# Optimization experiments

Hardware: AMD Instinct MI355X
Metric: run time of the kernel (lower is better)

## Reference

```python
import jax, jax.numpy as jnp
import numpy as np
import math

B, H, S, D, P = 1, 8, 512, 64, 32  # batch, heads, seq, d_k, proj_dim


def setup_inputs() -> dict:
    key = jax.random.key(0)
    ks = jax.random.split(key, 9)
    mu = math.log(math.sqrt(2.0 / D))  # PositiveLinear raw init mean

    def raw(k):
        return mu + 0.2 * jax.random.normal(k, (D, D), jnp.float32)

    return dict(
        q=jax.random.normal(ks[0], (B, H, S, D), jnp.float32),
        k=jax.random.normal(ks[1], (B, H, S, D), jnp.float32),
        v=jax.random.normal(ks[2], (B, H, S, D), jnp.float32),
        sq_raw1=raw(ks[3]), sq_b1=jnp.zeros((D,), jnp.float32),
        sq_raw2=raw(ks[4]), sq_b2=jnp.zeros((D,), jnp.float32),
        sk_raw1=raw(ks[5]), sk_b1=jnp.zeros((D,), jnp.float32),
        sk_raw2=raw(ks[6]), sk_b2=jnp.zeros((D,), jnp.float32),
        Wh=jax.random.normal(ks[7], (P, D), jnp.float32) / jnp.sqrt(jnp.float32(D)),
        Wv=jax.random.normal(ks[8], (P, D), jnp.float32) / jnp.sqrt(jnp.float32(D)),
    )


def _icnn(x, r1, b1, r2, b2):
    # Input-convex net: positive weights via softplus, softplus activations.
    z = jax.nn.softplus(x @ jax.nn.softplus(r1).T + b1)
    z = jax.nn.softplus(z @ jax.nn.softplus(r2).T + b2)
    return z.sum(-1)  # scalar convex score per token: [B,H,S]


def reference(q, k, v, sq_raw1, sq_b1, sq_raw2, sq_b2,
              sk_raw1, sk_b1, sk_raw2, sk_b2, Wh, Wv):
    f_q = _icnn(q, sq_raw1, sq_b1, sq_raw2, sq_b2)  # [B,H,S]
    g_k = _icnn(k, sk_raw1, sk_b1, sk_raw2, sk_b2)  # [B,H,S]
    phi_q = jnp.exp(q @ Wh.T)  # [B,H,S,P]
    phi_k = jnp.exp(k @ Wh.T)  # [B,H,S,P]
    scores = jnp.einsum('bhsr,bhtr->bhst', phi_q, phi_k)  # [B,H,S,S], strictly positive
    s_ij = f_q[..., :, None] + g_k[..., None, :] + jnp.log(scores)  # [B,H,S,S]
    u = v @ Wv.T  # [B,H,S,P] (index t)
    Sz = s_ij.shape[-1]
    # y[bhsp] = logsumexp_t(s_ij[bhst] + u[bhtp]) - log S, computed without the 5D tensor:
    m1 = jax.lax.stop_gradient(jnp.max(s_ij, axis=-1, keepdims=True))  # [B,H,S,1]
    m2 = jax.lax.stop_gradient(jnp.max(u, axis=2, keepdims=True))      # [B,H,1,P]
    acc = jnp.einsum('bhst,bhtp->bhsp', jnp.exp(s_ij - m1), jnp.exp(u - m2))
    y = jnp.log(acc) + m1 + m2 - jnp.log(jnp.float32(Sz))
    return y  # [B,H,S,P]
```

## Files before the change

kernel.cpp:

```cpp
#include <hip/hip_runtime.h>
#include <math.h>

#define HH 8
#define SS 512
#define DD 64
#define PP 32


__device__ __forceinline__ float softplusf(float x) {
    if (x > 20.f) return x;
    return log1pf(__expf(x));
}

__global__ __launch_bounds__(256) void csm_prep(
    const float* __restrict__ sq1, const float* __restrict__ sq2,
    const float* __restrict__ sk1, const float* __restrict__ sk2,
    const float* __restrict__ Wh, const float* __restrict__ Wv,
    float* __restrict__ wbuf)
{
    int idx = blockIdx.x * 256 + threadIdx.x;
    if (idx < 16384) {
        int m = idx >> 12, r = idx & 4095;
        int i = r >> 6, j = r & 63;
        const float* src = (m == 0) ? sq1 : (m == 1) ? sq2 : (m == 2) ? sk1 : sk2;
        wbuf[idx] = softplusf(src[j * 64 + i]);
    } else if (idx < 18432) {
        int r = idx - 16384; int i = r >> 5, p = r & 31;
        wbuf[idx] = Wh[p * 64 + i];
    } else if (idx < 20480) {
        int r = idx - 18432; int i = r >> 5, p = r & 31;
        wbuf[idx] = Wv[p * 64 + i];
    }
}

__global__ __launch_bounds__(256) void csm_token3(
    const float* __restrict__ q, const float* __restrict__ k, const float* __restrict__ v,
    const float* __restrict__ sq_b1, const float* __restrict__ sq_b2,
    const float* __restrict__ sk_b1, const float* __restrict__ sk_b2,
    const float* __restrict__ wbuf,
    float* __restrict__ fq, float* __restrict__ gk, float* __restrict__ gkpart,
    float* __restrict__ phiq, float* __restrict__ phik, float* __restrict__ uexp)
{
    __shared__ float xs[32 * 68];
    __shared__ float wb[64 * 68];
    __shared__ float wh[64 * 36];
    __shared__ float part[32 * 17];
    __shared__ float bb1[64], bb2[64];

    const int bx   = blockIdx.x;
    const int role = bx >> 7;
    const int sub  = bx & 127;
    const int g0   = sub * 32;
    const int tid  = threadIdx.x;
    const int tr = tid >> 4, tc = tid & 15;
    const int m0 = tr * 2, n0 = tc * 4, p0 = tc * 2;

    const float* xin = (role == 0) ? q : (role == 1) ? k : v;

    const float4* xsrc = (const float4*)(xin + g0 * 64);
    #pragma unroll
    for (int c = 0; c < 2; ++c) {
        int idx4 = tid + c * 256;
        int t = idx4 >> 4, ic = (idx4 & 15) * 4;
        *(float4*)&xs[t * 68 + ic] = xsrc[idx4];
    }
    const float4* whsrc = (const float4*)(wbuf + ((role == 2) ? 18432 : 16384));
    #pragma unroll
    for (int c = 0; c < 2; ++c) {
        int idx4 = tid + c * 256;
        int i = idx4 >> 3, pc = (idx4 & 7) * 4;
        *(float4*)&wh[i * 36 + pc] = whsrc[idx4];
    }
    if (role < 2) {
        const float4* w1src = (const float4*)(wbuf + (role == 0 ? 0 : 8192));
        #pragma unroll
        for (int c = 0; c < 4; ++c) {
            int idx4 = tid + c * 256;
            int i = idx4 >> 4, jc = (idx4 & 15) * 4;
            *(float4*)&wb[i * 68 + jc] = w1src[idx4];
        }
        if (tid < 64)       bb1[tid]      = (role == 0 ? sq_b1 : sk_b1)[tid];
        else if (tid < 128) bb2[tid - 64] = (role == 0 ? sq_b2 : sk_b2)[tid - 64];
    }
    __syncthreads();

    if (role == 2) {
        float acc[2][2] = {{0.f,0.f},{0.f,0.f}};
        #pragma unroll
        for (int kc = 0; kc < 16; ++kc) {
            const int i0 = kc * 4;
            float4 xv[2]; float2 hv[4];
            xv[0] = *(const float4*)&xs[(m0 + 0) * 68 + i0];
            xv[1] = *(const float4*)&xs[(m0 + 1) * 68 + i0];
            #pragma unroll
            for (int kk = 0; kk < 4; ++kk) hv[kk] = *(const float2*)&wh[(i0 + kk) * 36 + p0];
            #pragma unroll
            for (int mm = 0; mm < 2; ++mm) {
                const float* xa = (const float*)&xv[mm];
                #pragma unroll
                for (int kk = 0; kk < 4; ++kk) {
                    acc[mm][0] += xa[kk] * hv[kk].x;
                    acc[mm][1] += xa[kk] * hv[kk].y;
                }
            }
        }
        #pragma unroll
        for (int mm = 0; mm < 2; ++mm) {
            float2 o; o.x = __expf(acc[mm][0]); o.y = __expf(acc[mm][1]);
            *(float2*)&uexp[(g0 + m0 + mm) * 32 + p0] = o;
        }
        return;
    }

    float acc[2][4], accp[2][2];
    #pragma unroll
    for (int mm = 0; mm < 2; ++mm) {
        #pragma unroll
        for (int j = 0; j < 4; ++j) acc[mm][j] = bb1[n0 + j];
        accp[mm][0] = 0.f; accp[mm][1] = 0.f;
    }
    #pragma unroll
    for (int kc = 0; kc < 16; ++kc) {
        const int i0 = kc * 4;
        float4 xv[2], wv[4]; float2 hv[4];
        xv[0] = *(const float4*)&xs[(m0 + 0) * 68 + i0];
        xv[1] = *(const float4*)&xs[(m0 + 1) * 68 + i0];
        #pragma unroll
        for (int kk = 0; kk < 4; ++kk) {
            wv[kk] = *(const float4*)&wb[(i0 + kk) * 68 + n0];
            hv[kk] = *(const float2*)&wh[(i0 + kk) * 36 + p0];
        }
        #pragma unroll
        for (int mm = 0; mm < 2; ++mm) {
            const float* xa = (const float*)&xv[mm];
            #pragma unroll
            for (int kk = 0; kk < 4; ++kk) {
                const float xmk = xa[kk];
                const float* wa = (const float*)&wv[kk];
                acc[mm][0] += xmk * wa[0];
                acc[mm][1] += xmk * wa[1];
                acc[mm][2] += xmk * wa[2];
                acc[mm][3] += xmk * wa[3];
                accp[mm][0] += xmk * hv[kk].x;
                accp[mm][1] += xmk * hv[kk].y;
            }
        }
    }
    float* phiout = (role == 0) ? phiq : phik;
    #pragma unroll
    for (int mm = 0; mm < 2; ++mm) {
        float2 o; o.x = __expf(accp[mm][0]); o.y = __expf(accp[mm][1]);
        *(float2*)&phiout[(g0 + m0 + mm) * 32 + p0] = o;
    }
    float z1v[2][4];
    #pragma unroll
    for (int mm = 0; mm < 2; ++mm)
        #pragma unroll
        for (int j = 0; j < 4; ++j) z1v[mm][j] = softplusf(acc[mm][j]);
    __syncthreads();
    #pragma unroll
    for (int mm = 0; mm < 2; ++mm)
        *(float4*)&xs[(m0 + mm) * 68 + n0] = *(float4*)&z1v[mm][0];
    {
        const float4* w2src = (const float4*)(wbuf + (role == 0 ? 4096 : 12288));
        #pragma unroll
        for (int c = 0; c < 4; ++c) {
            int idx4 = tid + c * 256;
            int i = idx4 >> 4, jc = (idx4 & 15) * 4;
            *(float4*)&wb[i * 68 + jc] = w2src[idx4];
        }
    }
    __syncthreads();

    float acc2[2][4];
    #pragma unroll
    for (int mm = 0; mm < 2; ++mm)
        #pragma unroll
        for (int j = 0; j < 4; ++j) acc2[mm][j] = bb2[n0 + j];
    #pragma unroll
    for (int kc = 0; kc < 16; ++kc) {
        const int i0 = kc * 4;
        float4 xv[2], wv[4];
        xv[0] = *(const float4*)&xs[(m0 + 0) * 68 + i0];
        xv[1] = *(const float4*)&xs[(m0 + 1) * 68 + i0];
        #pragma unroll
        for (int kk = 0; kk < 4; ++kk) wv[kk] = *(const float4*)&wb[(i0 + kk) * 68 + n0];
        #pragma unroll
        for (int mm = 0; mm < 2; ++mm) {
            const float* xa = (const float*)&xv[mm];
            #pragma unroll
            for (int kk = 0; kk < 4; ++kk) {
                const float xmk = xa[kk];
                const float* wa = (const float*)&wv[kk];
                acc2[mm][0] += xmk * wa[0];
                acc2[mm][1] += xmk * wa[1];
                acc2[mm][2] += xmk * wa[2];
                acc2[mm][3] += xmk * wa[3];
            }
        }
    }
    #pragma unroll
    for (int mm = 0; mm < 2; ++mm) {
        float s = softplusf(acc2[mm][0]) + softplusf(acc2[mm][1])
                + softplusf(acc2[mm][2]) + softplusf(acc2[mm][3]);
        part[(m0 + mm) * 17 + tc] = s;
    }
    __syncthreads();
    if (tid < 32) {
        float s = 0.f;
        #pragma unroll
        for (int c = 0; c < 16; ++c) s += part[tid * 17 + c];
        if (role == 0) fq[g0 + tid] = s;
        else           gk[g0 + tid] = s;
        if (role == 1) {
            float mx = s;
            #pragma unroll
            for (int off = 16; off >= 1; off >>= 1)
                mx = fmaxf(mx, __shfl_xor(mx, off, 32));
            if (tid == 0) gkpart[sub] = mx;
        }
    }
}

__global__ __launch_bounds__(256) void csm_reduceM(
    const float* __restrict__ gk, const float* __restrict__ gkpart,
    const float* __restrict__ phik, const float* __restrict__ uexp,
    float* __restrict__ Mpart, float* __restrict__ Gbuf)
{
    __shared__ float wls[128];
    __shared__ float pk[128 * 36];
    __shared__ float wu[128 * 36];

    const int h     = blockIdx.x >> 2;
    const int chunk = blockIdx.x & 3;
    const int tid   = threadIdx.x;
    const int t0    = chunk * 128;

    float G = gkpart[h * 16];
    #pragma unroll
    for (int i = 1; i < 16; ++i) G = fmaxf(G, gkpart[h * 16 + i]);
    if (chunk == 0 && tid == 0) Gbuf[h] = G;

    if (tid < 128) wls[tid] = __expf(gk[h * SS + t0 + tid] - G);
    __syncthreads();

    const float4* psrc = (const float4*)(phik + (h * SS + t0) * PP);
    const float4* usrc = (const float4*)(uexp + (h * SS + t0) * PP);
    #pragma unroll
    for (int c = 0; c < 4; ++c) {
        int idx4 = tid + c * 256;
        int t = idx4 >> 3, pc = (idx4 & 7) * 4;
        *(float4*)&pk[t * 36 + pc] = psrc[idx4];
        float4 uv = usrc[idx4];
        float w = wls[t];
        uv.x *= w; uv.y *= w; uv.z *= w; uv.w *= w;
        *(float4*)&wu[t * 36 + pc] = uv;
    }
    __syncthreads();

    const int r0 = (tid >> 5) * 4, p = tid & 31;
    float macc[4] = {0.f, 0.f, 0.f, 0.f};
    for (int t = 0; t < 128; ++t) {
        const float wup = wu[t * 36 + p];
        const float4 pv = *(const float4*)&pk[t * 36 + r0];
        macc[0] += pv.x * wup;
        macc[1] += pv.y * wup;
        macc[2] += pv.z * wup;
        macc[3] += pv.w * wup;
    }
    float* mp = Mpart + blockIdx.x * 1024;
    #pragma unroll
    for (int rr = 0; rr < 4; ++rr)
        mp[(r0 + rr) * 32 + p] = macc[rr];
}

__global__ __launch_bounds__(256) void csm_out(
    const float* __restrict__ fq, const float* __restrict__ phiq,
    const float* __restrict__ Mpart, const float* __restrict__ Gbuf,
    float* __restrict__ y)
{
    __shared__ float Ms[32 * 36];
    __shared__ float pqs[8 * 32];
    __shared__ float fqs[8];

    const int bx = blockIdx.x;
    const int s0 = bx * 8;
    const int h  = bx >> 6;
    const int tid = threadIdx.x;

    {
        const int e = tid * 4;
        const float* base = Mpart + h * 4 * 1024 + e;
        float4 a = *(const float4*)(base);
        float4 b = *(const float4*)(base + 1024);
        float4 c = *(const float4*)(base + 2048);
        float4 d = *(const float4*)(base + 3072);
        float4 s;
        s.x = a.x + b.x + c.x + d.x;
        s.y = a.y + b.y + c.y + d.y;
        s.z = a.z + b.z + c.z + d.z;
        s.w = a.w + b.w + c.w + d.w;
        *(float4*)&Ms[(tid >> 3) * 36 + (tid & 7) * 4] = s;
    }
    pqs[tid] = phiq[s0 * 32 + tid];
    if (tid < 8) fqs[tid] = fq[s0 + tid];
    __syncthreads();

    const int si = tid >> 5, p = tid & 31;
    float acc = 0.f;
    #pragma unroll
    for (int rc = 0; rc < 8; ++rc) {
        const float4 pq = *(const float4*)&pqs[si * 32 + rc * 4];
        acc += pq.x * Ms[(rc * 4 + 0) * 36 + p];
        acc += pq.y * Ms[(rc * 4 + 1) * 36 + p];
        acc += pq.z * Ms[(rc * 4 + 2) * 36 + p];
        acc += pq.w * Ms[(rc * 4 + 3) * 36 + p];
    }
    const float LOG_S = 6.2383246250395078f;
    y[(s0 + si) * 32 + p] = __logf(acc) + fqs[si] + Gbuf[h] - LOG_S;
}

extern "C" void kernel_launch(void* const* d_in, const int* in_sizes, int n_in,
                              void* d_out, int out_size, void* d_ws, size_t ws_size,
                              hipStream_t stream) {
    (void)in_sizes; (void)n_in; (void)out_size; (void)ws_size;
    const float* q       = (const float*)d_in[0];
    const float* k       = (const float*)d_in[1];
    const float* v       = (const float*)d_in[2];
    const float* sq_raw1 = (const float*)d_in[3];
    const float* sq_b1   = (const float*)d_in[4];
    const float* sq_raw2 = (const float*)d_in[5];
    const float* sq_b2   = (const float*)d_in[6];
    const float* sk_raw1 = (const float*)d_in[7];
    const float* sk_b1   = (const float*)d_in[8];
    const float* sk_raw2 = (const float*)d_in[9];
    const float* sk_b2   = (const float*)d_in[10];
    const float* Wh      = (const float*)d_in[11];
    const float* Wv      = (const float*)d_in[12];
    float* y = (float*)d_out;

    float* ws     = (float*)d_ws;
    float* wbuf   = ws;
    float* fq     = ws + 20480;
    float* gk     = ws + 24576;
    float* gkpart = ws + 28672;
    float* Gbuf   = ws + 28800;
    float* phiq   = ws + 28928;
    float* phik   = ws + 160000;
    float* uexp   = ws + 291072;
    float* Mpart  = ws + 422144;

    csm_prep<<<80, 256, 0, stream>>>(sq_raw1, sq_raw2, sk_raw1, sk_raw2, Wh, Wv, wbuf);
    csm_token3<<<384, 256, 0, stream>>>(q, k, v, sq_b1, sq_b2, sk_b1, sk_b2,
                                        wbuf, fq, gk, gkpart, phiq, phik, uexp);
    csm_reduceM<<<32, 256, 0, stream>>>(gk, gkpart, phik, uexp, Mpart, Gbuf);
    csm_out<<<512, 256, 0, stream>>>(fq, phiq, Mpart, Gbuf, y);
}
```

Measured before the change: 102.7 us.

## Halve token tile, double grid sizes, and split reduceM into more chunks

The token kernel now handles 16 tokens per block instead of 32 (768 blocks) and preloads both ICNN weight matrices into separate shared buffers, which removes one barrier and the weight reload between layers. The per-token row sum now uses wave shuffles instead of a shared-memory partial array. The gk max moves into reduceM, which computes it per block from gk directly, and reduceM splits each head into 16 chunks (128 blocks) instead of 4. The aim is more parallelism on a GPU with many CUs, at the cost of more shared memory per block, redundant max computation, and csm_out summing 16 partials instead of 4.

New measurement: 105.2 us. +2.4%, slower.

```diff
diff --git a/kernel.cpp b/kernel.cpp
--- a/kernel.cpp
+++ b/kernel.cpp
@@ -33,51 +33,55 @@
     }
 }
 
-__global__ __launch_bounds__(256) void csm_token3(
+__global__ __launch_bounds__(256) void csm_token4(
     const float* __restrict__ q, const float* __restrict__ k, const float* __restrict__ v,
     const float* __restrict__ sq_b1, const float* __restrict__ sq_b2,
     const float* __restrict__ sk_b1, const float* __restrict__ sk_b2,
     const float* __restrict__ wbuf,
-    float* __restrict__ fq, float* __restrict__ gk, float* __restrict__ gkpart,
+    float* __restrict__ fq, float* __restrict__ gk,
     float* __restrict__ phiq, float* __restrict__ phik, float* __restrict__ uexp)
 {
-    __shared__ float xs[32 * 68];
-    __shared__ float wb[64 * 68];
-    __shared__ float wh[64 * 36];
-    __shared__ float part[32 * 17];
+    __shared__ float xs [16 * 68];
+    __shared__ float z1s[16 * 68];
+    __shared__ float wb1[64 * 68];
+    __shared__ float wb2[64 * 68];
+    __shared__ float wh [64 * 36];
     __shared__ float bb1[64], bb2[64];
 
     const int bx   = blockIdx.x;
-    const int role = bx >> 7;
-    const int sub  = bx & 127;
-    const int g0   = sub * 32;
+    const int role = bx >> 8;
+    const int sub  = bx & 255;
+    const int g0   = sub * 16;
     const int tid  = threadIdx.x;
-    const int tr = tid >> 4, tc = tid & 15;
-    const int m0 = tr * 2, n0 = tc * 4, p0 = tc * 2;
+    const int m0   = tid >> 4;
+    const int tc   = tid & 15;
+    const int n0   = tc * 4;
+    const int p0   = tc * 2;
 
     const float* xin = (role == 0) ? q : (role == 1) ? k : v;
 
-    const float4* xsrc = (const float4*)(xin + g0 * 64);
-    #pragma unroll
-    for (int c = 0; c < 2; ++c) {
-        int idx4 = tid + c * 256;
-        int t = idx4 >> 4, ic = (idx4 & 15) * 4;
-        *(float4*)&xs[t * 68 + ic] = xsrc[idx4];
-    }
-    const float4* whsrc = (const float4*)(wbuf + ((role == 2) ? 18432 : 16384));
-    #pragma unroll
-    for (int c = 0; c < 2; ++c) {
-        int idx4 = tid + c * 256;
-        int i = idx4 >> 3, pc = (idx4 & 7) * 4;
-        *(float4*)&wh[i * 36 + pc] = whsrc[idx4];
+    {
+        const float4* xsrc = (const float4*)(xin + g0 * 64);
+        *(float4*)&xs[m0 * 68 + tc * 4] = xsrc[tid];
+    }
+    {
+        const float4* whsrc = (const float4*)(wbuf + ((role == 2) ? 18432 : 16384));
+        #pragma unroll
+        for (int c = 0; c < 2; ++c) {
+            int idx4 = tid + c * 256;
+            int i = idx4 >> 3, pc = (idx4 & 7) * 4;
+            *(float4*)&wh[i * 36 + pc] = whsrc[idx4];
+        }
     }
     if (role < 2) {
         const float4* w1src = (const float4*)(wbuf + (role == 0 ? 0 : 8192));
+        const float4* w2src = (const float4*)(wbuf + (role == 0 ? 4096 : 12288));
         #pragma unroll
         for (int c = 0; c < 4; ++c) {
             int idx4 = tid + c * 256;
             int i = idx4 >> 4, jc = (idx4 & 15) * 4;
-            *(float4*)&wb[i * 68 + jc] = w1src[idx4];
+            *(float4*)&wb1[i * 68 + jc] = w1src[idx4];
+            *(float4*)&wb2[i * 68 + jc] = w2src[idx4];
         }
         if (tid < 64)       bb1[tid]      = (role == 0 ? sq_b1 : sk_b1)[tid];
         else if (tid < 128) bb2[tid - 64] = (role == 0 ? sq_b2 : sk_b2)[tid - 64];
@@ -85,193 +89,128 @@
     __syncthreads();
 
     if (role == 2) {
-        float acc[2][2] = {{0.f,0.f},{0.f,0.f}};
+        float a0 = 0.f, a1 = 0.f;
         #pragma unroll
         for (int kc = 0; kc < 16; ++kc) {
             const int i0 = kc * 4;
-            float4 xv[2]; float2 hv[4];
-            xv[0] = *(const float4*)&xs[(m0 + 0) * 68 + i0];
-            xv[1] = *(const float4*)&xs[(m0 + 1) * 68 + i0];
+            float4 xv = *(const float4*)&xs[m0 * 68 + i0];
+            const float* xa = (const float*)&xv;
             #pragma unroll
-            for (int kk = 0; kk < 4; ++kk) hv[kk] = *(const float2*)&wh[(i0 + kk) * 36 + p0];
-            #pragma unroll
-            for (int mm = 0; mm < 2; ++mm) {
-                const float* xa = (const float*)&xv[mm];
-                #pragma unroll
-                for (int kk = 0; kk < 4; ++kk) {
-                    acc[mm][0] += xa[kk] * hv[kk].x;
-                    acc[mm][1] += xa[kk] * hv[kk].y;
-                }
+            for (int kk = 0; kk < 4; ++kk) {
+                float2 hv = *(const float2*)&wh[(i0 + kk) * 36 + p0];
+                a0 += xa[kk] * hv.x;
+                a1 += xa[kk] * hv.y;
             }
         }
-        #pragma unroll
-        for (int mm = 0; mm < 2; ++mm) {
-            float2 o; o.x = __expf(acc[mm][0]); o.y = __expf(acc[mm][1]);
-            *(float2*)&uexp[(g0 + m0 + mm) * 32 + p0] = o;
-        }
+        float2 o; o.x = __expf(a0); o.y = __expf(a1);
+        *(float2*)&uexp[(g0 + m0) * 32 + p0] = o;
         return;
     }
 
-    float acc[2][4], accp[2][2];
-    #pragma unroll
-    for (int mm = 0; mm < 2; ++mm) {
-        #pragma unroll
-        for (int j = 0; j < 4; ++j) acc[mm][j] = bb1[n0 + j];
-        accp[mm][0] = 0.f; accp[mm][1] = 0.f;
-    }
+    float4 acc = *(const float4*)&bb1[n0];
+    float ap0 = 0.f, ap1 = 0.f;
     #pragma unroll
     for (int kc = 0; kc < 16; ++kc) {
         const int i0 = kc * 4;
-        float4 xv[2], wv[4]; float2 hv[4];
-        xv[0] = *(const float4*)&xs[(m0 + 0) * 68 + i0];
-        xv[1] = *(const float4*)&xs[(m0 + 1) * 68 + i0];
+        float4 xv = *(const float4*)&xs[m0 * 68 + i0];
+        const float* xa = (const float*)&xv;
         #pragma unroll
         for (int kk = 0; kk < 4; ++kk) {
-            wv[kk] = *(const float4*)&wb[(i0 + kk) * 68 + n0];
-            hv[kk] = *(const float2*)&wh[(i0 + kk) * 36 + p0];
-        }
-        #pragma unroll
-        for (int mm = 0; mm < 2; ++mm) {
-            const float* xa = (const float*)&xv[mm];
-            #pragma unroll
-            for (int kk = 0; kk < 4; ++kk) {
-                const float xmk = xa[kk];
-                const float* wa = (const float*)&wv[kk];
-                acc[mm][0] += xmk * wa[0];
-                acc[mm][1] += xmk * wa[1];
-                acc[mm][2] += xmk * wa[2];
-                acc[mm][3] += xmk * wa[3];
-                accp[mm][0] += xmk * hv[kk].x;
-                accp[mm][1] += xmk * hv[kk].y;
-            }
-        }
-    }
-    float* phiout = (role == 0) ? phiq : phik;
-    #pragma unroll
-    for (int mm = 0; mm < 2; ++mm) {
-        float2 o; o.x = __expf(accp[mm][0]); o.y = __expf(accp[mm][1]);
-        *(float2*)&phiout[(g0 + m0 + mm) * 32 + p0] = o;
-    }
-    float z1v[2][4];
-    #pragma unroll
-    for (int mm = 0; mm < 2; ++mm)
-        #pragma unroll
-        for (int j = 0; j < 4; ++j) z1v[mm][j] = softplusf(acc[mm][j]);
-    __syncthreads();
-    #pragma unroll
-    for (int mm = 0; mm < 2; ++mm)
-        *(float4*)&xs[(m0 + mm) * 68 + n0] = *(float4*)&z1v[mm][0];
-    {
-        const float4* w2src = (const float4*)(wbuf + (role == 0 ? 4096 : 12288));
-        #pragma unroll
-        for (int c = 0; c < 4; ++c) {
-            int idx4 = tid + c * 256;
-            int i = idx4 >> 4, jc = (idx4 & 15) * 4;
-            *(float4*)&wb[i * 68 + jc] = w2src[idx4];
-        }
-    }
-    __syncthreads();
-
-    float acc2[2][4];
-    #pragma unroll
-    for (int mm = 0; mm < 2; ++mm)
-        #pragma unroll
-        for (int j = 0; j < 4; ++j) acc2[mm][j] = bb2[n0 + j];
+            float4 wv = *(const float4*)&wb1[(i0 + kk) * 68 + n0];
+            float2 hv = *(const float2*)&wh[(i0 + kk) * 36 + p0];
+            const float xk = xa[kk];
+            acc.x += xk * wv.x; acc.y += xk * wv.y;
+            acc.z += xk * wv.z; acc.w += xk * wv.w;
+            ap0   += xk * hv.x; ap1   += xk * hv.y;
+        }
+    }
+    {
+        float* phiout = (role == 0) ? phiq : phik;
+        float2 o; o.x = __expf(ap0); o.y = __expf(ap1);
+        *(float2*)&phiout[(g0 + m0) * 32 + p0] = o;
+    }
+    {
+        float4 z1;
+        z1.x = softplusf(acc.x); z1.y = softplusf(acc.y);
+        z1.z = softplusf(acc.z); z1.w = softplusf(acc.w);
+        *(float4*)&z1s[m0 * 68 + n0] = z1;
+    }
+    __syncthreads();
+
+    float4 a2 = *(const float4*)&bb2[n0];
     #pragma unroll
     for (int kc = 0; kc < 16; ++kc) {
         const int i0 = kc * 4;
-        float4 xv[2], wv[4];
-        xv[0] = *(const float4*)&xs[(m0 + 0) * 68 + i0];
-        xv[1] = *(const float4*)&xs[(m0 + 1) * 68 + i0];
-        #pragma unroll
-        for (int kk = 0; kk < 4; ++kk) wv[kk] = *(const float4*)&wb[(i0 + kk) * 68 + n0];
-        #pragma unroll
-        for (int mm = 0; mm < 2; ++mm) {
-            const float* xa = (const float*)&xv[mm];
-            #pragma unroll
-            for (int kk = 0; kk < 4; ++kk) {
-                const float xmk = xa[kk];
-                const float* wa = (const float*)&wv[kk];
-                acc2[mm][0] += xmk * wa[0];
-                acc2[mm][1] += xmk * wa[1];
-                acc2[mm][2] += xmk * wa[2];
-                acc2[mm][3] += xmk * wa[3];
-            }
-        }
-    }
-    #pragma unroll
-    for (int mm = 0; mm < 2; ++mm) {
-        float s = softplusf(acc2[mm][0]) + softplusf(acc2[mm][1])
-                + softplusf(acc2[mm][2]) + softplusf(acc2[mm][3]);
-        part[(m0 + mm) * 17 + tc] = s;
-    }
-    __syncthreads();
-    if (tid < 32) {
-        float s = 0.f;
-        #pragma unroll
-        for (int c = 0; c < 16; ++c) s += part[tid * 17 + c];
-        if (role == 0) fq[g0 + tid] = s;
-        else           gk[g0 + tid] = s;
-        if (role == 1) {
-            float mx = s;
-            #pragma unroll
-            for (int off = 16; off >= 1; off >>= 1)
-                mx = fmaxf(mx, __shfl_xor(mx, off, 32));
-            if (tid == 0) gkpart[sub] = mx;
-        }
+        float4 xv = *(const float4*)&z1s[m0 * 68 + i0];
+        const float* xa = (const float*)&xv;
+        #pragma unroll
+        for (int kk = 0; kk < 4; ++kk) {
+            float4 wv = *(const float4*)&wb2[(i0 + kk) * 68 + n0];
+            const float xk = xa[kk];
+            a2.x += xk * wv.x; a2.y += xk * wv.y;
+            a2.z += xk * wv.z; a2.w += xk * wv.w;
+        }
+    }
+    float s = softplusf(a2.x) + softplusf(a2.y) + softplusf(a2.z) + softplusf(a2.w);
+    s += __shfl_xor(s, 1);
+    s += __shfl_xor(s, 2);
+    s += __shfl_xor(s, 4);
+    s += __shfl_xor(s, 8);
+    if (tc == 0) {
+        if (role == 0) fq[g0 + m0] = s;
+        else           gk[g0 + m0] = s;
     }
 }
 
 __global__ __launch_bounds__(256) void csm_reduceM(
-    const float* __restrict__ gk, const float* __restrict__ gkpart,
+    const float* __restrict__ gk,
     const float* __restrict__ phik, const float* __restrict__ uexp,
     float* __restrict__ Mpart, float* __restrict__ Gbuf)
 {
-    __shared__ float wls[128];
-    __shared__ float pk[128 * 36];
-    __shared__ float wu[128 * 36];
-
-    const int h     = blockIdx.x >> 2;
-    const int chunk = blockIdx.x & 3;
+    __shared__ float pk[32 * 36];
+    __shared__ float wu[32 * 36];
+    __shared__ float wls[32];
+    __shared__ float gred[4];
+
+    const int h     = blockIdx.x >> 4;
+    const int chunk = blockIdx.x & 15;
     const int tid   = threadIdx.x;
-    const int t0    = chunk * 128;
-
-    float G = gkpart[h * 16];
-    #pragma unroll
-    for (int i = 1; i < 16; ++i) G = fmaxf(G, gkpart[h * 16 + i]);
+    const int t0    = chunk * 32;
+
+    float g = fmaxf(gk[h * SS + tid], gk[h * SS + 256 + tid]);
+    #pragma unroll
+    for (int off = 1; off < 64; off <<= 1) g = fmaxf(g, __shfl_xor(g, off));
+    if ((tid & 63) == 0) gred[tid >> 6] = g;
+    __syncthreads();
+    const float G = fmaxf(fmaxf(gred[0], gred[1]), fmaxf(gred[2], gred[3]));
     if (chunk == 0 && tid == 0) Gbuf[h] = G;
-
-    if (tid < 128) wls[tid] = __expf(gk[h * SS + t0 + tid] - G);
-    __syncthreads();
-
-    const float4* psrc = (const float4*)(phik + (h * SS + t0) * PP);
-    const float4* usrc = (const float4*)(uexp + (h * SS + t0) * PP);
-    #pragma unroll
-    for (int c = 0; c < 4; ++c) {
-        int idx4 = tid + c * 256;
-        int t = idx4 >> 3, pc = (idx4 & 7) * 4;
-        *(float4*)&pk[t * 36 + pc] = psrc[idx4];
-        float4 uv = usrc[idx4];
-        float w = wls[t];
-        uv.x *= w; uv.y *= w; uv.z *= w; uv.w *= w;
-        *(float4*)&wu[t * 36 + pc] = uv;
-    }
-    __syncthreads();
-
-    const int r0 = (tid >> 5) * 4, p = tid & 31;
-    float macc[4] = {0.f, 0.f, 0.f, 0.f};
-    for (int t = 0; t < 128; ++t) {
-        const float wup = wu[t * 36 + p];
+    if (tid < 32) wls[tid] = __expf(gk[h * SS + t0 + tid] - G);
+
+    {
+        const float4* psrc = (const float4*)(phik + (h * SS + t0) * PP);
+        const float4* usrc = (const float4*)(uexp + (h * SS + t0) * PP);
+        int t = tid >> 3, pc = (tid & 7) * 4;
+        *(float4*)&pk[t * 36 + pc] = psrc[tid];
+        *(float4*)&wu[t * 36 + pc] = usrc[tid];
+    }
+    __syncthreads();
+
+    const int r0 = ((tid >> 5) & 7) * 4, p = tid & 31;
+    float m0_ = 0.f, m1_ = 0.f, m2_ = 0.f, m3_ = 0.f;
+    #pragma unroll
+    for (int t = 0; t < 32; ++t) {
+        const float wup = wu[t * 36 + p] * wls[t];
         const float4 pv = *(const float4*)&pk[t * 36 + r0];
-        macc[0] += pv.x * wup;
-        macc[1] += pv.y * wup;
-        macc[2] += pv.z * wup;
-        macc[3] += pv.w * wup;
+        m0_ += pv.x * wup;
+        m1_ += pv.y * wup;
+        m2_ += pv.z * wup;
+        m3_ += pv.w * wup;
     }
     float* mp = Mpart + blockIdx.x * 1024;
-    #pragma unroll
-    for (int rr = 0; rr < 4; ++rr)
-        mp[(r0 + rr) * 32 + p] = macc[rr];
+    mp[(r0 + 0) * 32 + p] = m0_;
+    mp[(r0 + 1) * 32 + p] = m1_;
+    mp[(r0 + 2) * 32 + p] = m2_;
+    mp[(r0 + 3) * 32 + p] = m3_;
 }
 
 __global__ __launch_bounds__(256) void csm_out(
@@ -289,17 +228,13 @@
     const int tid = threadIdx.x;
 
     {
-        const int e = tid * 4;
-        const float* base = Mpart + h * 4 * 1024 + e;
-        float4 a = *(const float4*)(base);
-        float4 b = *(const float4*)(base + 1024);
-        float4 c = *(const float4*)(base + 2048);
-        float4 d = *(const float4*)(base + 3072);
-        float4 s;
-        s.x = a.x + b.x + c.x + d.x;
-        s.y = a.y + b.y + c.y + d.y;
-        s.z = a.z + b.z + c.z + d.z;
-        s.w = a.w + b.w + c.w + d.w;
+        const float* base = Mpart + h * 16 * 1024 + tid * 4;
+        float4 s = *(const float4*)base;
+        #pragma unroll
+        for (int c = 1; c < 16; ++c) {
+            float4 a = *(const float4*)(base + c * 1024);
+            s.x += a.x; s.y += a.y; s.z += a.z; s.w += a.w;
+        }
         *(float4*)&Ms[(tid >> 3) * 36 + (tid & 7) * 4] = s;
     }
     pqs[tid] = phiq[s0 * 32 + tid];
@@ -343,16 +278,15 @@
     float* wbuf   = ws;
     float* fq     = ws + 20480;
     float* gk     = ws + 24576;
-    float* gkpart = ws + 28672;
-    float* Gbuf   = ws + 28800;
-    float* phiq   = ws + 28928;
-    float* phik   = ws + 160000;
-    float* uexp   = ws + 291072;
-    float* Mpart  = ws + 422144;
+    float* Gbuf   = ws + 28672;
+    float* phiq   = ws + 28800;
+    float* phik   = ws + 159872;
+    float* uexp   = ws + 290944;
+    float* Mpart  = ws + 422016;
 
     csm_prep<<<80, 256, 0, stream>>>(sq_raw1, sq_raw2, sk_raw1, sk_raw2, Wh, Wv, wbuf);
-    csm_token3<<<384, 256, 0, stream>>>(q, k, v, sq_b1, sq_b2, sk_b1, sk_b2,
-                                        wbuf, fq, gk, gkpart, phiq, phik, uexp);
-    csm_reduceM<<<32, 256, 0, stream>>>(gk, gkpart, phik, uexp, Mpart, Gbuf);
+    csm_token4<<<768, 256, 0, stream>>>(q, k, v, sq_b1, sq_b2, sk_b1, sk_b2,
+                                        wbuf, fq, gk, phiq, phik, uexp);
+    csm_reduceM<<<128, 256, 0, stream>>>(gk, phik, uexp, Mpart, Gbuf);
     csm_out<<<512, 256, 0, stream>>>(fq, phiq, Mpart, Gbuf, y);
 }
```
